# Performance work log

Hardware: AMD Instinct MI355X
Metric: run time of the kernel (lower is better)

The kernel has to match this reference:

```python
import jax, jax.numpy as jnp
import numpy as np

NUM_CLASSES = 10
OUTPUT_DIM = 128
HIDDEN_DIM = 64


def setup_inputs() -> dict:
    key = jax.random.key(0)
    k1, k2, k3, k4, k5, k6 = jax.random.split(key, 6)
    B, S, F = 16, 4096, 512
    X_support = jax.random.normal(k1, (B, S, F), dtype=jnp.float32)
    y_support = jax.random.randint(k2, (B, S), 0, NUM_CLASSES, dtype=jnp.int32)
    # MLP params: Linear(6, HIDDEN) -> GELU -> Linear(HIDDEN, OUTPUT)
    w1 = jax.random.normal(k3, (6, HIDDEN_DIM), dtype=jnp.float32) * (1.0 / np.sqrt(6.0))
    b1 = jax.random.normal(k4, (HIDDEN_DIM,), dtype=jnp.float32) * 0.01
    w2 = jax.random.normal(k5, (HIDDEN_DIM, OUTPUT_DIM), dtype=jnp.float32) * (1.0 / np.sqrt(HIDDEN_DIM))
    b2 = jax.random.normal(k6, (OUTPUT_DIM,), dtype=jnp.float32) * 0.01
    return {"X_support": X_support, "y_support": y_support,
            "w1": w1, "b1": b1, "w2": w2, "b2": b2}


def _feature_target_stats(X, y):
    """Vectorized equivalent of FeatureTargetStatsEncoder per-(batch,feature) loops.
    X: [B, S, F] float, y: [B, S] int class labels. Returns stats [B, F, 6]."""
    B, S, F = X.shape
    missing_rate = jnp.isnan(X).astype(X.dtype).mean(axis=1)           # [B, F]
    Xc = jnp.nan_to_num(X, nan=0.0)
    gmean = Xc.mean(axis=1)                                            # [B, F]
    variance = Xc.var(axis=1)                                          # biased (unbiased=False)
    absX = jnp.abs(Xc)
    mean_abs = absX.mean(axis=1)
    max_abs = absX.max(axis=1)
    # unique_ratio: count distinct values per (b, f) via sort + diff
    xs = jnp.sort(Xc, axis=1)
    n_unique = 1.0 + (jnp.diff(xs, axis=1) != 0).astype(Xc.dtype).sum(axis=1)
    unique_ratio = n_unique / S
    # classification target score: between-class variance / overall variance
    onehot = jax.nn.one_hot(y, NUM_CLASSES, dtype=Xc.dtype)            # [B, S, C]
    counts = onehot.sum(axis=1)                                        # [B, C]
    csum = jnp.einsum('bsc,bsf->bcf', onehot, Xc)                      # [B, C, F]
    cmean = csum / jnp.maximum(counts, 1.0)[:, :, None]
    dev2 = (cmean - gmean[:, None, :]) ** 2
    between = (counts[:, :, None] * dev2).sum(axis=1) / jnp.maximum(counts.sum(axis=1), 1.0)[:, None]
    target_score = between / jnp.maximum(variance, 1e-6)
    stats = jnp.stack([target_score, missing_rate, unique_ratio,
                       variance, mean_abs, max_abs], axis=-1)          # [B, F, 6]
    return jnp.nan_to_num(stats, nan=0.0, posinf=0.0, neginf=0.0)


def reference(X_support, y_support, w1, b1, w2, b2):
    stats = _feature_target_stats(X_support, y_support)                # [B, F, 6]
    h = jax.nn.gelu(stats @ w1 + b1, approximate=False)               # exact GELU like nn.GELU()
    return h @ w2 + b2                                                 # [B, F, OUTPUT_DIM]
```

## Files before the change

kernel.cpp:

```cpp
#include <hip/hip_runtime.h>
#include <math.h>

#define NS 4096
#define NF 512
#define NB 16
#define NC 10
#define HSIZE 8192
#define HMASK 8191
#define HEMPTY 0xFFFFFFFFu

__global__ void count_classes_kernel(const int* __restrict__ y, float* __restrict__ counts) {
    __shared__ int hist[NC];
    const int b = blockIdx.x;
    if (threadIdx.x < NC) hist[threadIdx.x] = 0;
    __syncthreads();
    for (int s = threadIdx.x; s < NS; s += blockDim.x)
        atomicAdd(&hist[y[b * NS + s]], 1);
    __syncthreads();
    if (threadIdx.x < NC) counts[b * NC + threadIdx.x] = (float)hist[threadIdx.x];
}

__device__ __forceinline__ float wave_reduce_add(float v) {
    #pragma unroll
    for (int off = 32; off > 0; off >>= 1) v += __shfl_down(v, off, 64);
    return v;
}
__device__ __forceinline__ float wave_reduce_max(float v) {
    #pragma unroll
    for (int off = 32; off > 0; off >>= 1) v = fmaxf(v, __shfl_down(v, off, 64));
    return v;
}

__launch_bounds__(256)
__global__ void fused_stats_mlp_kernel(const float* __restrict__ X,
                                       const int* __restrict__ y,
                                       const float* __restrict__ counts,
                                       const float* __restrict__ w1,
                                       const float* __restrict__ b1,
                                       const float* __restrict__ w2,
                                       const float* __restrict__ b2,
                                       float* __restrict__ out) {
    __shared__ unsigned int hash[HSIZE];
    __shared__ float red[4][16];
    __shared__ float stats_s[6];
    __shared__ float h_s[64];

    const int w = blockIdx.x;
    const int g = (w & 7) * 1024 + (w >> 3);
    const int b = g >> 9;
    const int f = g & (NF - 1);
    const int tid = threadIdx.x;

    #pragma unroll
    for (int i = 0; i < HSIZE / 256; i++) hash[tid + i * 256] = HEMPTY;
    __syncthreads();

    const float* Xp = X + (size_t)b * NS * NF + f;
    const int*   yp = y + b * NS;

    float sum = 0.f, sumsq = 0.f, sumabs = 0.f, maxabs = 0.f, nancnt = 0.f, uniq = 0.f;
    float csum[NC];
    #pragma unroll
    for (int c = 0; c < NC; c++) csum[c] = 0.f;

    #pragma unroll
    for (int k0 = 0; k0 < 16; k0 += 8) {
        float xv[8]; int yv[8];
        #pragma unroll
        for (int k = 0; k < 8; k++) {
            const int s = (k0 + k) * 256 + tid;
            xv[k] = Xp[(size_t)s * NF];
            yv[k] = yp[s];
        }
        #pragma unroll
        for (int k = 0; k < 8; k++) {
            float x = xv[k];
            if (x != x) { nancnt += 1.f; x = 0.f; }
            sum += x;
            sumsq = fmaf(x, x, sumsq);
            const float a = fabsf(x);
            sumabs += a;
            maxabs = fmaxf(maxabs, a);
            const int yc = yv[k];
            #pragma unroll
            for (int c = 0; c < NC; c++) csum[c] += (yc == c) ? x : 0.f;
            unsigned int pat = __float_as_uint(x);
            if (pat == 0x80000000u) pat = 0u;
            unsigned int slot = (pat * 2654435761u) >> 19;
            for (;;) {
                const unsigned int old = atomicCAS(&hash[slot], HEMPTY, pat);
                if (old == HEMPTY) { uniq += 1.f; break; }
                if (old == pat) break;
                slot = (slot + 1) & HMASK;
            }
        }
    }

    sum    = wave_reduce_add(sum);
    sumsq  = wave_reduce_add(sumsq);
    sumabs = wave_reduce_add(sumabs);
    nancnt = wave_reduce_add(nancnt);
    uniq   = wave_reduce_add(uniq);
    maxabs = wave_reduce_max(maxabs);
    #pragma unroll
    for (int c = 0; c < NC; c++) csum[c] = wave_reduce_add(csum[c]);

    const int wave = tid >> 6, lane = tid & 63;
    if (lane == 0) {
        red[wave][0] = sum;    red[wave][1] = sumsq; red[wave][2] = sumabs;
        red[wave][3] = nancnt; red[wave][4] = uniq;  red[wave][5] = maxabs;
        #pragma unroll
        for (int c = 0; c < NC; c++) red[wave][6 + c] = csum[c];
    }
    __syncthreads();

    if (tid == 0) {
        float t[16];
        #pragma unroll
        for (int v = 0; v < 16; v++) t[v] = red[0][v];
        #pragma unroll
        for (int wv = 1; wv < 4; wv++) {
            #pragma unroll
            for (int v = 0; v < 16; v++) {
                if (v == 5) t[v] = fmaxf(t[v], red[wv][v]);
                else        t[v] += red[wv][v];
            }
        }
        const float invS = 1.f / (float)NS;
        const float gmean    = t[0] * invS;
        const float variance = fmaxf(t[1] * invS - gmean * gmean, 0.f);
        const float mean_abs = t[2] * invS;
        const float missing  = t[3] * invS;
        const float n_unique = t[4];
        const float max_abs  = t[5];
        float between = 0.f;
        #pragma unroll
        for (int c = 0; c < NC; c++) {
            const float cnt = counts[b * NC + c];
            const float cm  = t[6 + c] / fmaxf(cnt, 1.f);
            const float d   = cm - gmean;
            between += cnt * d * d;
        }
        between *= invS;
        const float target = between / fmaxf(variance, 1e-6f);
        float st[6] = { target, missing, n_unique * invS, variance, mean_abs, max_abs };
        #pragma unroll
        for (int i = 0; i < 6; i++) {
            float v = st[i];
            if (!(fabsf(v) < INFINITY)) v = 0.f;
            stats_s[i] = v;
        }
    }
    __syncthreads();

    if (tid < 64) {
        float z = b1[tid];
        #pragma unroll
        for (int i = 0; i < 6; i++) z = fmaf(stats_s[i], w1[i * 64 + tid], z);
        h_s[tid] = 0.5f * z * (1.f + erff(z * 0.70710678118654752440f));
    }
    __syncthreads();
    if (tid < 128) {
        float o = b2[tid];
        #pragma unroll
        for (int j = 0; j < 64; j++) o = fmaf(h_s[j], w2[j * 128 + tid], o);
        out[(size_t)g * 128 + tid] = o;
    }
}

extern "C" void kernel_launch(void* const* d_in, const int* in_sizes, int n_in,
                              void* d_out, int out_size, void* d_ws, size_t ws_size,
                              hipStream_t stream) {
    const float* X  = (const float*)d_in[0];
    const int*   y  = (const int*)d_in[1];
    const float* w1 = (const float*)d_in[2];
    const float* b1 = (const float*)d_in[3];
    const float* w2 = (const float*)d_in[4];
    const float* b2 = (const float*)d_in[5];
    float* out    = (float*)d_out;
    float* counts = (float*)d_ws;

    count_classes_kernel<<<NB, 256, 0, stream>>>(y, counts);
    fused_stats_mlp_kernel<<<NB * NF, 256, 0, stream>>>(X, y, counts, w1, b1, w2, b2, out);
}
```

Baseline: 354.5 us.

## Use shared-memory atomics for class sums and split hashing into a separate phase

Per-class sums are no longer held as ten per-thread registers with wave reductions. Each element now does a shared-memory atomicAdd into a per-wave class table, and the NaN-cleaned bit patterns are kept in registers. The hash table then reuses the same shared buffer: it is cleared with vectorized uint4 stores and filled in a second phase using quadratic probing, and the reduction scratch is aliased into it too. Launch bounds now request 5 blocks per CU. The goal is lower register pressure, higher occupancy and less shuffle work, at the cost of extra barriers, LDS atomic contention on the ten class bins, and 16 more registers holding patterns.

Result: slower. 460.5 us (+29.9%).

```diff
diff --git a/kernel.cpp b/kernel.cpp
--- a/kernel.cpp
+++ b/kernel.cpp
@@ -31,7 +31,7 @@
     return v;
 }
 
-__launch_bounds__(256)
+__launch_bounds__(256, 5)
 __global__ void fused_stats_mlp_kernel(const float* __restrict__ X,
                                        const int* __restrict__ y,
                                        const float* __restrict__ counts,
@@ -40,28 +40,24 @@
                                        const float* __restrict__ w2,
                                        const float* __restrict__ b2,
                                        float* __restrict__ out) {
-    __shared__ unsigned int hash[HSIZE];
-    __shared__ float red[4][16];
-    __shared__ float stats_s[6];
-    __shared__ float h_s[64];
+    __shared__ __align__(16) unsigned int hash[HSIZE];
 
     const int w = blockIdx.x;
     const int g = (w & 7) * 1024 + (w >> 3);
     const int b = g >> 9;
     const int f = g & (NF - 1);
     const int tid = threadIdx.x;
+    const int wave = tid >> 6, lane = tid & 63;
 
-    #pragma unroll
-    for (int i = 0; i < HSIZE / 256; i++) hash[tid + i * 256] = HEMPTY;
+    float* csumtab = (float*)hash;
+    if (tid < 4 * NC) csumtab[tid] = 0.f;
     __syncthreads();
 
     const float* Xp = X + (size_t)b * NS * NF + f;
     const int*   yp = y + b * NS;
 
-    float sum = 0.f, sumsq = 0.f, sumabs = 0.f, maxabs = 0.f, nancnt = 0.f, uniq = 0.f;
-    float csum[NC];
-    #pragma unroll
-    for (int c = 0; c < NC; c++) csum[c] = 0.f;
+    float sum = 0.f, sumsq = 0.f, sumabs = 0.f, maxabs = 0.f, nancnt = 0.f;
+    unsigned int pat[16];
 
     #pragma unroll
     for (int k0 = 0; k0 < 16; k0 += 8) {
@@ -81,20 +77,44 @@
             const float a = fabsf(x);
             sumabs += a;
             maxabs = fmaxf(maxabs, a);
-            const int yc = yv[k];
-            #pragma unroll
-            for (int c = 0; c < NC; c++) csum[c] += (yc == c) ? x : 0.f;
-            unsigned int pat = __float_as_uint(x);
-            if (pat == 0x80000000u) pat = 0u;
-            unsigned int slot = (pat * 2654435761u) >> 19;
-            for (;;) {
-                const unsigned int old = atomicCAS(&hash[slot], HEMPTY, pat);
-                if (old == HEMPTY) { uniq += 1.f; break; }
-                if (old == pat) break;
-                slot = (slot + 1) & HMASK;
-            }
+            atomicAdd(&csumtab[wave * NC + yv[k]], x);
+            unsigned int p = __float_as_uint(x);
+            if (p == 0x80000000u) p = 0u;
+            pat[k0 + k] = p;
         }
     }
+    __syncthreads();
+
+    float my_csum = 0.f;
+    if (tid < NC)
+        my_csum = csumtab[tid] + csumtab[NC + tid] +
+                  csumtab[2 * NC + tid] + csumtab[3 * NC + tid];
+    __syncthreads();
+
+    uint4* h4 = (uint4*)hash;
+    const uint4 e4 = make_uint4(HEMPTY, HEMPTY, HEMPTY, HEMPTY);
+    #pragma unroll
+    for (int i = 0; i < HSIZE / 4 / 256; i++) h4[i * 256 + tid] = e4;
+    __syncthreads();
+
+    float uniq = 0.f;
+    #pragma unroll
+    for (int k = 0; k < 16; k++) {
+        const unsigned int p = pat[k];
+        unsigned int slot = (p * 2654435761u) >> 19;
+        unsigned int step = 0;
+        for (;;) {
+            const unsigned int old = atomicCAS(&hash[slot], HEMPTY, p);
+            if (old == HEMPTY) { uniq += 1.f; break; }
+            if (old == p) break;
+            slot = (slot + (++step)) & HMASK;
+        }
+    }
+    __syncthreads();
+
+    float (*red)[8] = (float(*)[8])hash;
+    float* stats_s  = (float*)hash + 64;
+    float* h_s      = (float*)hash + 128;
 
     sum    = wave_reduce_add(sum);
     sumsq  = wave_reduce_add(sumsq);
@@ -102,53 +122,47 @@
     nancnt = wave_reduce_add(nancnt);
     uniq   = wave_reduce_add(uniq);
     maxabs = wave_reduce_max(maxabs);
-    #pragma unroll
-    for (int c = 0; c < NC; c++) csum[c] = wave_reduce_add(csum[c]);
 
-    const int wave = tid >> 6, lane = tid & 63;
     if (lane == 0) {
         red[wave][0] = sum;    red[wave][1] = sumsq; red[wave][2] = sumabs;
         red[wave][3] = nancnt; red[wave][4] = uniq;  red[wave][5] = maxabs;
-        #pragma unroll
-        for (int c = 0; c < NC; c++) red[wave][6 + c] = csum[c];
     }
     __syncthreads();
 
-    if (tid == 0) {
-        float t[16];
+    if (tid < 64) {
+        float t0 = 0.f, t1 = 0.f, t2 = 0.f, t3 = 0.f, t4 = 0.f, t5 = 0.f;
         #pragma unroll
-        for (int v = 0; v < 16; v++) t[v] = red[0][v];
-        #pragma unroll
-        for (int wv = 1; wv < 4; wv++) {
-            #pragma unroll
-            for (int v = 0; v < 16; v++) {
-                if (v == 5) t[v] = fmaxf(t[v], red[wv][v]);
-                else        t[v] += red[wv][v];
-            }
+        for (int wv = 0; wv < 4; wv++) {
+            t0 += red[wv][0]; t1 += red[wv][1]; t2 += red[wv][2];
+            t3 += red[wv][3]; t4 += red[wv][4];
+            t5 = fmaxf(t5, red[wv][5]);
         }
         const float invS = 1.f / (float)NS;
-        const float gmean    = t[0] * invS;
-        const float variance = fmaxf(t[1] * invS - gmean * gmean, 0.f);
-        const float mean_abs = t[2] * invS;
-        const float missing  = t[3] * invS;
-        const float n_unique = t[4];
-        const float max_abs  = t[5];
+        const float gmean    = t0 * invS;
+        const float variance = fmaxf(t1 * invS - gmean * gmean, 0.f);
+        const float mean_abs = t2 * invS;
+        const float missing  = t3 * invS;
+        const float n_unique = t4;
+        const float max_abs  = t5;
         float between = 0.f;
         #pragma unroll
         for (int c = 0; c < NC; c++) {
+            const float csv = __shfl(my_csum, c, 64);
             const float cnt = counts[b * NC + c];
-            const float cm  = t[6 + c] / fmaxf(cnt, 1.f);
+            const float cm  = csv / fmaxf(cnt, 1.f);
             const float d   = cm - gmean;
-            between += cnt * d * d;
+            between = fmaf(cnt * d, d, between);
         }
         between *= invS;
         const float target = between / fmaxf(variance, 1e-6f);
-        float st[6] = { target, missing, n_unique * invS, variance, mean_abs, max_abs };
-        #pragma unroll
-        for (int i = 0; i < 6; i++) {
-            float v = st[i];
-            if (!(fabsf(v) < INFINITY)) v = 0.f;
-            stats_s[i] = v;
+        if (lane == 0) {
+            float st[6] = { target, missing, n_unique * invS, variance, mean_abs, max_abs };
+            #pragma unroll
+            for (int i = 0; i < 6; i++) {
+                float v = st[i];
+                if (!(fabsf(v) < INFINITY)) v = 0.f;
+                stats_s[i] = v;
+            }
         }
     }
     __syncthreads();
```

## Transpose X into workspace so per-feature blocks read contiguous float4 columns

Applied to the files above, without the earlier changes.

Adds a tiled shared-memory transpose kernel that writes X as [B,F,S] into the workspace. The stats kernel then reads each feature's samples as contiguous float4 vectors instead of strided scalar loads across NF. This costs an extra full read and write of X (128 MB each way) in exchange for coalesced reads. It only runs when the workspace is large enough, otherwise the old kernel is used.

After: 378.1 us. 1.07x slower.

```diff
diff --git a/kernel.cpp b/kernel.cpp
--- a/kernel.cpp
+++ b/kernel.cpp
@@ -8,6 +8,7 @@
 #define HSIZE 8192
 #define HMASK 8191
 #define HEMPTY 0xFFFFFFFFu
+#define WS_XT_OFF 1024
 
 __global__ void count_classes_kernel(const int* __restrict__ y, float* __restrict__ counts) {
     __shared__ int hist[NC];
@@ -29,6 +30,178 @@
     #pragma unroll
     for (int off = 32; off > 0; off >>= 1) v = fmaxf(v, __shfl_down(v, off, 64));
     return v;
+}
+
+__launch_bounds__(256)
+__global__ void transpose_kernel(const float* __restrict__ X, float* __restrict__ XT) {
+    __shared__ float t[64][65];
+    const int b  = blockIdx.x;
+    const int s0 = blockIdx.y * 64;
+    const int f0 = blockIdx.z * 64;
+    const int tid = threadIdx.x;
+
+    const int fi = (tid & 15) * 4;
+    const int si = tid >> 4;
+    const float* Xb = X + ((size_t)b * NS + s0) * NF + f0;
+    #pragma unroll
+    for (int i = 0; i < 4; i++) {
+        const int s = si + 16 * i;
+        const float4 v = *(const float4*)(Xb + (size_t)s * NF + fi);
+        t[s][fi + 0] = v.x; t[s][fi + 1] = v.y;
+        t[s][fi + 2] = v.z; t[s][fi + 3] = v.w;
+    }
+    __syncthreads();
+
+    const int sj = (tid & 15) * 4;
+    const int fj = tid >> 4;
+    float* XTb = XT + ((size_t)b * NF + f0) * NS + s0;
+    #pragma unroll
+    for (int i = 0; i < 4; i++) {
+        const int f = fj + 16 * i;
+        float4 v;
+        v.x = t[sj + 0][f]; v.y = t[sj + 1][f];
+        v.z = t[sj + 2][f]; v.w = t[sj + 3][f];
+        *(float4*)(XTb + (size_t)f * NS + sj) = v;
+    }
+}
+
+__launch_bounds__(256)
+__global__ void fused_stats_mlp_xt(const float* __restrict__ XT,
+                                   const int* __restrict__ y,
+                                   const float* __restrict__ counts,
+                                   const float* __restrict__ w1,
+                                   const float* __restrict__ b1,
+                                   const float* __restrict__ w2,
+                                   const float* __restrict__ b2,
+                                   float* __restrict__ out) {
+    __shared__ unsigned int hash[HSIZE];
+    __shared__ float red[4][16];
+    __shared__ float stats_s[6];
+    __shared__ float h_s[64];
+
+    const int w = blockIdx.x;
+    const int g = (w & 7) * 1024 + (w >> 3);
+    const int b = g >> 9;
+    const int f = g & (NF - 1);
+    const int tid = threadIdx.x;
+
+    #pragma unroll
+    for (int i = 0; i < HSIZE / 256; i++) hash[tid + i * 256] = HEMPTY;
+    __syncthreads();
+
+    const float4* Xc4 = (const float4*)(XT + ((size_t)b * NF + f) * NS);
+    const int4*   yp4 = (const int4*)(y + (size_t)b * NS);
+
+    float sum = 0.f, sumsq = 0.f, sumabs = 0.f, maxabs = 0.f, nancnt = 0.f, uniq = 0.f;
+    float csum[NC];
+    #pragma unroll
+    for (int c = 0; c < NC; c++) csum[c] = 0.f;
+
+    float4 xv[4]; int4 yv[4];
+    #pragma unroll
+    for (int k = 0; k < 4; k++) {
+        xv[k] = Xc4[k * 256 + tid];
+        yv[k] = yp4[k * 256 + tid];
+    }
+
+    #pragma unroll
+    for (int k = 0; k < 4; k++) {
+        const float xe[4] = { xv[k].x, xv[k].y, xv[k].z, xv[k].w };
+        const int   ye[4] = { yv[k].x, yv[k].y, yv[k].z, yv[k].w };
+        #pragma unroll
+        for (int j = 0; j < 4; j++) {
+            float x = xe[j];
+            if (x != x) { nancnt += 1.f; x = 0.f; }
+            sum += x;
+            sumsq = fmaf(x, x, sumsq);
+            const float a = fabsf(x);
+            sumabs += a;
+            maxabs = fmaxf(maxabs, a);
+            const int yc = ye[j];
+            #pragma unroll
+            for (int c = 0; c < NC; c++) csum[c] += (yc == c) ? x : 0.f;
+            unsigned int pat = __float_as_uint(x);
+            if (pat == 0x80000000u) pat = 0u;
+            unsigned int slot = (pat * 2654435761u) >> 19;
+            for (;;) {
+                const unsigned int old = atomicCAS(&hash[slot], HEMPTY, pat);
+                if (old == HEMPTY) { uniq += 1.f; break; }
+                if (old == pat) break;
+                slot = (slot + 1) & HMASK;
+            }
+        }
+    }
+
+    sum    = wave_reduce_add(sum);
+    sumsq  = wave_reduce_add(sumsq);
+    sumabs = wave_reduce_add(sumabs);
+    nancnt = wave_reduce_add(nancnt);
+    uniq   = wave_reduce_add(uniq);
+    maxabs = wave_reduce_max(maxabs);
+    #pragma unroll
+    for (int c = 0; c < NC; c++) csum[c] = wave_reduce_add(csum[c]);
+
+    const int wave = tid >> 6, lane = tid & 63;
+    if (lane == 0) {
+        red[wave][0] = sum;    red[wave][1] = sumsq; red[wave][2] = sumabs;
+        red[wave][3] = nancnt; red[wave][4] = uniq;  red[wave][5] = maxabs;
+        #pragma unroll
+        for (int c = 0; c < NC; c++) red[wave][6 + c] = csum[c];
+    }
+    __syncthreads();
+
+    if (tid == 0) {
+        float t[16];
+        #pragma unroll
+        for (int v = 0; v < 16; v++) t[v] = red[0][v];
+        #pragma unroll
+        for (int wv = 1; wv < 4; wv++) {
+            #pragma unroll
+            for (int v = 0; v < 16; v++) {
+                if (v == 5) t[v] = fmaxf(t[v], red[wv][v]);
+                else        t[v] += red[wv][v];
+            }
+        }
+        const float invS = 1.f / (float)NS;
+        const float gmean    = t[0] * invS;
+        const float variance = fmaxf(t[1] * invS - gmean * gmean, 0.f);
+        const float mean_abs = t[2] * invS;
+        const float missing  = t[3] * invS;
+        const float n_unique = t[4];
+        const float max_abs  = t[5];
+        float between = 0.f;
+        #pragma unroll
+        for (int c = 0; c < NC; c++) {
+            const float cnt = counts[b * NC + c];
+            const float cm  = t[6 + c] / fmaxf(cnt, 1.f);
+            const float d   = cm - gmean;
+            between += cnt * d * d;
+        }
+        between *= invS;
+        const float target = between / fmaxf(variance, 1e-6f);
+        float st[6] = { target, missing, n_unique * invS, variance, mean_abs, max_abs };
+        #pragma unroll
+        for (int i = 0; i < 6; i++) {
+            float v = st[i];
+            if (!(fabsf(v) < INFINITY)) v = 0.f;
+            stats_s[i] = v;
+        }
+    }
+    __syncthreads();
+
+    if (tid < 64) {
+        float z = b1[tid];
+        #pragma unroll
+        for (int i = 0; i < 6; i++) z = fmaf(stats_s[i], w1[i * 64 + tid], z);
+        h_s[tid] = 0.5f * z * (1.f + erff(z * 0.70710678118654752440f));
+    }
+    __syncthreads();
+    if (tid < 128) {
+        float o = b2[tid];
+        #pragma unroll
+        for (int j = 0; j < 64; j++) o = fmaf(h_s[j], w2[j * 128 + tid], o);
+        out[(size_t)g * 128 + tid] = o;
+    }
 }
 
 __launch_bounds__(256)
@@ -181,5 +354,13 @@
     float* counts = (float*)d_ws;
 
     count_classes_kernel<<<NB, 256, 0, stream>>>(y, counts);
-    fused_stats_mlp_kernel<<<NB * NF, 256, 0, stream>>>(X, y, counts, w1, b1, w2, b2, out);
-}
+
+    const size_t xt_bytes = (size_t)NB * NF * NS * sizeof(float);
+    if (ws_size >= xt_bytes + WS_XT_OFF) {
+        float* XT = (float*)((char*)d_ws + WS_XT_OFF);
+        transpose_kernel<<<dim3(NB, NS / 64, NF / 64), 256, 0, stream>>>(X, XT);
+        fused_stats_mlp_xt<<<NB * NF, 256, 0, stream>>>(XT, y, counts, w1, b1, w2, b2, out);
+    } else {
+        fused_stats_mlp_kernel<<<NB * NF, 256, 0, stream>>>(X, y, counts, w1, b1, w2, b2, out);
+    }
+}
```
